# Kernel optimization log

Hardware: AMD Instinct MI355X
Metric: run time of the kernel (lower is better)

## Reference

```python
import jax, jax.numpy as jnp
import numpy as np

N_NODES = 100000
N_EDGES = 1600000
IN_FEAT = 64
OUT_FEAT = 64
NUM_RELS = 8


def setup_inputs() -> dict:
    key = jax.random.key(0)
    k1, k2, k3, k4, k5, k6 = jax.random.split(key, 6)
    feat = jax.random.normal(k1, (N_NODES, IN_FEAT), dtype=jnp.float32)
    norm = jax.random.uniform(k2, (N_EDGES, 1), dtype=jnp.float32)
    # nn.init.uniform_(weight, -1/sqrt(in_feat), 1/sqrt(in_feat))
    bound = 1.0 / np.sqrt(IN_FEAT)
    weight = jax.random.uniform(k3, (NUM_RELS, IN_FEAT, OUT_FEAT), dtype=jnp.float32,
                                minval=-bound, maxval=bound)
    etypes = jax.random.randint(k4, (N_EDGES,), 0, NUM_RELS, dtype=jnp.int64 if jax.config.jax_enable_x64 else jnp.int32)
    src = jax.random.randint(k5, (N_EDGES,), 0, N_NODES, dtype=jnp.int32)
    dst = jax.random.randint(k6, (N_EDGES,), 0, N_NODES, dtype=jnp.int32)
    return {"feat": feat, "norm": norm, "weight": weight,
            "etypes": etypes, "src": src, "dst": dst}


def reference(feat, norm, weight, etypes, src, dst):
    # Original: per-relation grouped matmul on gathered src features, scale by
    # norm, scatter-sum to dst. Matmul distributes over the gather, so we
    # transform all N node features by all R relation weights once (dense GEMM),
    # then gather the right (relation, src) row per edge — same math, fully
    # vectorized, avoids per-edge [in,out] weight gathers.
    transformed = jnp.einsum('ni,rio->rno', feat, weight)   # [R, N, out]
    msg = transformed[etypes, src]                           # [E, out]
    msg = msg * norm                                         # norm broadcasts [E,1]
    out = jax.ops.segment_sum(msg, dst, num_segments=feat.shape[0])  # [N, out]
    return out
```

## Files before the change

kernel.cpp:

```cpp
#include <hip/hip_runtime.h>
#include <hip/hip_bf16.h>

#define N_NODES 100000
#define N_EDGES 1600000
#define IN_FEAT 64
#define OUT_FEAT 64
#define NUM_RELS 8

#define BSHIFT 7
#define BSZ 128
#define NB ((N_NODES + BSZ - 1) / BSZ)
#define CHUNK 4096
#define NCHUNK ((N_EDGES + CHUNK - 1) / CHUNK)
#define PSTR 392
#define MAXBUCK 2944

typedef __attribute__((ext_vector_type(8))) short short8;
typedef __attribute__((ext_vector_type(8))) unsigned short ushort8;
typedef __attribute__((ext_vector_type(4))) float f32x4;

static __device__ __forceinline__ unsigned short f2bf(float x) {
    unsigned u = __float_as_uint(x);
    unsigned r = (u + 0x7FFFu + ((u >> 16) & 1u)) >> 16;
    return (unsigned short)r;
}
static __device__ __forceinline__ float bf2f(unsigned short h) {
    return __uint_as_float(((unsigned)h) << 16);
}
static __device__ __forceinline__ float bflo(unsigned v) { return __uint_as_float(v << 16); }
static __device__ __forceinline__ float bfhi(unsigned v) { return __uint_as_float(v & 0xFFFF0000u); }

__global__ __launch_bounds__(256) void k_prep(const float* __restrict__ W,
                                              unsigned short* __restrict__ Wt) {
    __shared__ float Wl[64 * 64];
    const int r = blockIdx.x, t = threadIdx.x;
    #pragma unroll
    for (int it = 0; it < 16; ++it) {
        int idx = it * 256 + t;
        Wl[idx] = W[(size_t)r * 4096 + idx];
    }
    __syncthreads();
    const int o = t >> 2, iq = t & 3;
    unsigned short tmp[16];
    #pragma unroll
    for (int k = 0; k < 16; ++k) tmp[k] = f2bf(Wl[(iq * 16 + k) * 64 + o]);
    ushort8* dst = (ushort8*)(Wt + ((size_t)r * 64 + o) * 64 + iq * 16);
    dst[0] = *(ushort8*)&tmp[0];
    dst[1] = *(ushort8*)&tmp[8];
}

__global__ __launch_bounds__(256) void k_transform(const float* __restrict__ feat,
                                                   const unsigned short* __restrict__ Wt,
                                                   unsigned short* __restrict__ trb) {
    __shared__ unsigned short Ft[64 * 72];
    __shared__ unsigned short Wtl[64 * 72];
    const int tid = threadIdx.x;
    const int n0b = blockIdx.x * 64;
    const int lane = tid & 63, w = tid >> 6;
    const int lr = lane & 15, lg = lane >> 4;

    #pragma unroll
    for (int it = 0; it < 4; ++it) {
        int m = it * 256 + tid;
        int row = m >> 4, c4 = m & 15;
        int gn = n0b + row;
        float4 v = make_float4(0.f, 0.f, 0.f, 0.f);
        if (gn < N_NODES) v = *(const float4*)(feat + (size_t)gn * IN_FEAT + c4 * 4);
        ushort4 sv;
        sv.x = f2bf(v.x); sv.y = f2bf(v.y); sv.z = f2bf(v.z); sv.w = f2bf(v.w);
        *(ushort4*)&Ft[row * 72 + c4 * 4] = sv;
    }

    for (int rel = 0; rel < NUM_RELS; ++rel) {
        __syncthreads();
        #pragma unroll
        for (int it = 0; it < 2; ++it) {
            int m = it * 256 + tid;
            int row = m >> 3, kq = m & 7;
            *(ushort8*)&Wtl[row * 72 + kq * 8] =
                *(const ushort8*)(Wt + (size_t)rel * 4096 + m * 8);
        }
        __syncthreads();

        short8 a0 = *(const short8*)&Ft[(16 * w + lr) * 72 + lg * 8];
        short8 a1 = *(const short8*)&Ft[(16 * w + lr) * 72 + 32 + lg * 8];

        #pragma unroll
        for (int nt = 0; nt < 4; ++nt) {
            short8 b0 = *(const short8*)&Wtl[(nt * 16 + lr) * 72 + lg * 8];
            short8 b1 = *(const short8*)&Wtl[(nt * 16 + lr) * 72 + 32 + lg * 8];
            f32x4 acc = {0.f, 0.f, 0.f, 0.f};
            acc = __builtin_amdgcn_mfma_f32_16x16x32_bf16(a0, b0, acc, 0, 0, 0);
            acc = __builtin_amdgcn_mfma_f32_16x16x32_bf16(a1, b1, acc, 0, 0, 0);
            #pragma unroll
            for (int j = 0; j < 4; ++j) {
                int row = n0b + 16 * w + lg * 4 + j;
                if (row < N_NODES)
                    trb[((size_t)rel * N_NODES + row) * OUT_FEAT + nt * 16 + lr] = f2bf(acc[j]);
            }
        }
    }
}

__device__ __forceinline__ int block_scan1024(int* arr, int* tmp) {
    const int t = threadIdx.x;
    const int i0 = t * 4;
    int v0 = arr[i0], v1 = arr[i0 + 1], v2 = arr[i0 + 2], v3 = arr[i0 + 3];
    int s = v0 + v1 + v2 + v3;
    tmp[t] = s;
    __syncthreads();
    for (int off = 1; off < 256; off <<= 1) {
        int x = (t >= off) ? tmp[t - off] : 0;
        __syncthreads();
        tmp[t] += x;
        __syncthreads();
    }
    int excl = tmp[t] - s;
    int total = tmp[255];
    arr[i0]     = excl;
    arr[i0 + 1] = excl + v0;
    arr[i0 + 2] = excl + v0 + v1;
    arr[i0 + 3] = excl + v0 + v1 + v2;
    __syncthreads();
    return total;
}

__global__ __launch_bounds__(256) void k_bhist(const int* __restrict__ dst,
                                               int* __restrict__ cnt_kb) {
    __shared__ int h[NB];
    const int k = blockIdx.x, t = threadIdx.x;
    for (int i = t; i < NB; i += 256) h[i] = 0;
    __syncthreads();
    const int e0 = k * CHUNK;
    #pragma unroll
    for (int i = 0; i < 16; ++i) {
        int e = e0 + t + i * 256;
        if (e < N_EDGES) atomicAdd(&h[dst[e] >> BSHIFT], 1);
    }
    __syncthreads();
    for (int i = t; i < NB; i += 256) cnt_kb[(size_t)k * NB + i] = h[i];
}

__global__ __launch_bounds__(256) void k_scan_bucket(const int* __restrict__ cnt_kb,
                                                     int* __restrict__ poff,
                                                     int* __restrict__ btot) {
    __shared__ int arr[1024];
    __shared__ int tmp[256];
    const int b = blockIdx.x, t = threadIdx.x;
    for (int i = t; i < 1024; i += 256)
        arr[i] = (i < NCHUNK) ? cnt_kb[(size_t)i * NB + b] : 0;
    __syncthreads();
    int total = block_scan1024(arr, tmp);
    for (int i = t; i < NCHUNK; i += 256) poff[(size_t)b * PSTR + i] = arr[i];
    if (t == 0) btot[b] = total;
}

__global__ __launch_bounds__(256) void k_scan_tot(const int* __restrict__ btot,
                                                  int* __restrict__ bbase) {
    __shared__ int arr[1024];
    __shared__ int tmp[256];
    const int t = threadIdx.x;
    for (int i = t; i < 1024; i += 256) arr[i] = (i < NB) ? btot[i] : 0;
    __syncthreads();
    block_scan1024(arr, tmp);
    for (int i = t; i < NB; i += 256) bbase[i] = arr[i];
    if (t == 0) bbase[NB] = N_EDGES;
}

__global__ __launch_bounds__(256) void k_bin(const int* __restrict__ etypes,
                                             const int* __restrict__ src,
                                             const int* __restrict__ dst,
                                             const float* __restrict__ norm,
                                             const int* __restrict__ poff,
                                             const int* __restrict__ bbase,
                                             int2* __restrict__ payload) {
    __shared__ int hist[1024];
    __shared__ int tmp[256];
    __shared__ int lcur[NB];
    __shared__ int goff[NB];
    __shared__ int2 ordered[CHUNK];
    __shared__ unsigned short bkt_of[CHUNK];
    const int k = blockIdx.x, t = threadIdx.x;
    const int e0 = k * CHUNK;
    const int cnt = min(CHUNK, N_EDGES - e0);

    for (int i = t; i < 1024; i += 256) hist[i] = 0;
    __syncthreads();
    #pragma unroll
    for (int i = 0; i < 16; ++i) {
        int e = e0 + t + i * 256;
        if (e < N_EDGES) atomicAdd(&hist[dst[e] >> BSHIFT], 1);
    }
    __syncthreads();
    block_scan1024(hist, tmp);
    for (int i = t; i < NB; i += 256) {
        int lb = hist[i];
        lcur[i] = lb;
        goff[i] = bbase[i] + poff[(size_t)i * PSTR + k] - lb;
    }
    __syncthreads();
    #pragma unroll
    for (int i = 0; i < 16; ++i) {
        int e = e0 + t + i * 256;
        if (e < N_EDGES) {
            int d = dst[e];
            int b = d >> BSHIFT;
            int pos = atomicAdd(&lcur[b], 1);
            int rowid = etypes[e] * N_NODES + src[e];
            ordered[pos] = make_int2(rowid | ((d & (BSZ - 1)) << 20), __float_as_int(norm[e]));
            bkt_of[pos] = (unsigned short)b;
        }
    }
    __syncthreads();
    for (int j = t; j < cnt; j += 256) {
        int b = bkt_of[j];
        payload[goff[b] + j] = ordered[j];
    }
}

__global__ __launch_bounds__(512) void k_agg(const unsigned short* __restrict__ trb,
                                             const int2* __restrict__ payload,
                                             const int* __restrict__ bbase,
                                             float* __restrict__ out) {
    __shared__ int2 pseg[MAXBUCK];
    __shared__ unsigned short sidx[MAXBUCK];
    __shared__ int cnt128[BSZ];
    __shared__ int scan_tmp[BSZ];
    __shared__ int ncur[BSZ];
    __shared__ int nbase[BSZ + 1];
    const int b = blockIdx.x, t = threadIdx.x;

    const int s0 = bbase[b], s1 = bbase[b + 1];
    const int cntb = s1 - s0;
    const int cstage = min(cntb, MAXBUCK);

    if (t < BSZ) cnt128[t] = 0;
    __syncthreads();

    for (int i = t; i < cstage; i += 512) {
        int2 p = payload[s0 + i];
        pseg[i] = p;
        atomicAdd(&cnt128[(p.x >> 20) & 127], 1);
    }
    __syncthreads();

    if (t < BSZ) scan_tmp[t] = cnt128[t];
    __syncthreads();
    for (int off = 1; off < BSZ; off <<= 1) {
        int x = 0;
        if (t < BSZ && t >= off) x = scan_tmp[t - off];
        __syncthreads();
        if (t < BSZ) scan_tmp[t] += x;
        __syncthreads();
    }
    if (t < BSZ) {
        int inc = scan_tmp[t];
        int exc = inc - cnt128[t];
        nbase[t] = exc;
        ncur[t] = exc;
        if (t == BSZ - 1) nbase[BSZ] = inc;
    }
    __syncthreads();

    for (int i = t; i < cstage; i += 512) {
        int ld = (pseg[i].x >> 20) & 127;
        int pos = atomicAdd(&ncur[ld], 1);
        sidx[pos] = (unsigned short)i;
    }
    __syncthreads();

    const int gg = t >> 3;
    const int q  = t & 7;
    const int n0g = b << BSHIFT;

    #pragma unroll
    for (int rr = 0; rr < 2; ++rr) {
        int r = gg + rr * 64;
        int j0 = nbase[r], j1 = nbase[r + 1];
        float a0 = 0.f, a1 = 0.f, a2 = 0.f, a3 = 0.f;
        float a4 = 0.f, a5 = 0.f, a6 = 0.f, a7 = 0.f;
        int j = j0;
        for (; j + 1 < j1; j += 2) {
            int2 pa = pseg[sidx[j]];
            int2 pb = pseg[sidx[j + 1]];
            uint4 ua = *(const uint4*)(trb + (size_t)(pa.x & 0xFFFFF) * OUT_FEAT + (q << 3));
            uint4 ub = *(const uint4*)(trb + (size_t)(pb.x & 0xFFFFF) * OUT_FEAT + (q << 3));
            float na = __int_as_float(pa.y);
            float nb_ = __int_as_float(pb.y);
            a0 += bflo(ua.x) * na; a1 += bfhi(ua.x) * na;
            a2 += bflo(ua.y) * na; a3 += bfhi(ua.y) * na;
            a4 += bflo(ua.z) * na; a5 += bfhi(ua.z) * na;
            a6 += bflo(ua.w) * na; a7 += bfhi(ua.w) * na;
            a0 += bflo(ub.x) * nb_; a1 += bfhi(ub.x) * nb_;
            a2 += bflo(ub.y) * nb_; a3 += bfhi(ub.y) * nb_;
            a4 += bflo(ub.z) * nb_; a5 += bfhi(ub.z) * nb_;
            a6 += bflo(ub.w) * nb_; a7 += bfhi(ub.w) * nb_;
        }
        if (j < j1) {
            int2 p = pseg[sidx[j]];
            uint4 u = *(const uint4*)(trb + (size_t)(p.x & 0xFFFFF) * OUT_FEAT + (q << 3));
            float nv = __int_as_float(p.y);
            a0 += bflo(u.x) * nv; a1 += bfhi(u.x) * nv;
            a2 += bflo(u.y) * nv; a3 += bfhi(u.y) * nv;
            a4 += bflo(u.z) * nv; a5 += bfhi(u.z) * nv;
            a6 += bflo(u.w) * nv; a7 += bfhi(u.w) * nv;
        }
        int n = n0g + r;
        if (n < N_NODES) {
            float* op = out + (size_t)n * OUT_FEAT + (q << 3);
            *(float4*)op       = make_float4(a0, a1, a2, a3);
            *(float4*)(op + 4) = make_float4(a4, a5, a6, a7);
        }
    }

    if (cntb > MAXBUCK) {
        __syncthreads();
        for (int i = MAXBUCK + t; i < cntb; i += 512) {
            int2 p = payload[s0 + i];
            int row = p.x & 0xFFFFF;
            int n = n0g + ((p.x >> 20) & 127);
            float nv = __int_as_float(p.y);
            if (n < N_NODES)
                for (int c = 0; c < OUT_FEAT; ++c)
                    atomicAdd(&out[(size_t)n * OUT_FEAT + c],
                              bf2f(trb[(size_t)row * OUT_FEAT + c]) * nv);
        }
    }
}

__global__ __launch_bounds__(256) void k_scatter(const unsigned short* __restrict__ trb,
                                                 const float* __restrict__ norm,
                                                 const int* __restrict__ etypes,
                                                 const int* __restrict__ src,
                                                 const int* __restrict__ dst,
                                                 float* __restrict__ out) {
    int gid = blockIdx.x * 256 + threadIdx.x;
    int e = gid >> 4;
    int q = gid & 15;
    if (e >= N_EDGES) return;
    float nv = norm[e];
    const unsigned short* rp = trb + ((size_t)etypes[e] * N_NODES + src[e]) * OUT_FEAT + q * 4;
    ushort4 u = *(const ushort4*)rp;
    float* op = out + (size_t)dst[e] * OUT_FEAT + q * 4;
    atomicAdd(op + 0, bf2f(u.x) * nv);
    atomicAdd(op + 1, bf2f(u.y) * nv);
    atomicAdd(op + 2, bf2f(u.z) * nv);
    atomicAdd(op + 3, bf2f(u.w) * nv);
}

__global__ __launch_bounds__(256) void k_direct(const float* __restrict__ feat,
                                                const float* __restrict__ W,
                                                const float* __restrict__ norm,
                                                const int* __restrict__ etypes,
                                                const int* __restrict__ src,
                                                const int* __restrict__ dst,
                                                float* __restrict__ out) {
    int gid = blockIdx.x * 256 + threadIdx.x;
    int e = gid >> 4;
    int q = gid & 15;
    if (e >= N_EDGES) return;
    float nv = norm[e];
    const float* fs = feat + (size_t)src[e] * IN_FEAT;
    const float* wp = W + (size_t)etypes[e] * 4096 + q * 4;
    float ax = 0.f, ay = 0.f, az = 0.f, aw = 0.f;
    #pragma unroll 8
    for (int i = 0; i < IN_FEAT; ++i) {
        float f = fs[i];
        float4 w = *(const float4*)(wp + i * OUT_FEAT);
        ax += f * w.x; ay += f * w.y; az += f * w.z; aw += f * w.w;
    }
    float* op = out + (size_t)dst[e] * OUT_FEAT + q * 4;
    atomicAdd(op + 0, ax * nv);
    atomicAdd(op + 1, ay * nv);
    atomicAdd(op + 2, az * nv);
    atomicAdd(op + 3, aw * nv);
}

extern "C" void kernel_launch(void* const* d_in, const int* in_sizes, int n_in,
                              void* d_out, int out_size, void* d_ws, size_t ws_size,
                              hipStream_t stream) {
    const float* feat   = (const float*)d_in[0];
    const float* norm   = (const float*)d_in[1];
    const float* W      = (const float*)d_in[2];
    const int*   etypes = (const int*)d_in[3];
    const int*   src    = (const int*)d_in[4];
    const int*   dst    = (const int*)d_in[5];
    float* out = (float*)d_out;

    const int ntiles = (N_NODES + 63) / 64;
    const int nscat  = (N_EDGES * 16) / 256;

    const size_t sz_tr    = (size_t)NUM_RELS * N_NODES * OUT_FEAT * 2;
    const size_t sz_wt    = (size_t)NUM_RELS * 64 * 64 * 2;
    const size_t sz_cnt   = (((size_t)NCHUNK * NB * 4) + 255) & ~(size_t)255;
    const size_t sz_poff  = (((size_t)NB * PSTR * 4) + 255) & ~(size_t)255;
    const size_t sz_btot  = 3328;
    const size_t sz_bbase = 3328;
    const size_t sz_pay   = (size_t)N_EDGES * 8;

    char* p = (char*)d_ws;
    unsigned short* trb = (unsigned short*)p;  p += sz_tr;
    unsigned short* wt  = (unsigned short*)p;  p += sz_wt;
    int*  cnt_kb  = (int*)p;                   p += sz_cnt;
    int*  poff    = (int*)p;                   p += sz_poff;
    int*  btot    = (int*)p;                   p += sz_btot;
    int*  bbase   = (int*)p;                   p += sz_bbase;
    int2* payload = (int2*)p;                  p += sz_pay;
    const size_t need = (size_t)(p - (char*)d_ws);

    if (ws_size >= need) {
        k_prep       <<<NUM_RELS, 256, 0, stream>>>(W, wt);
        k_transform  <<<ntiles, 256, 0, stream>>>(feat, wt, trb);
        k_bhist      <<<NCHUNK, 256, 0, stream>>>(dst, cnt_kb);
        k_scan_bucket<<<NB,     256, 0, stream>>>(cnt_kb, poff, btot);
        k_scan_tot   <<<1,      256, 0, stream>>>(btot, bbase);
        k_bin        <<<NCHUNK, 256, 0, stream>>>(etypes, src, dst, norm, poff, bbase, payload);
        k_agg        <<<NB,     512, 0, stream>>>(trb, payload, bbase, out);
    } else if (ws_size >= sz_tr + sz_wt) {
        hipMemsetAsync(d_out, 0, (size_t)out_size * sizeof(float), stream);
        k_prep     <<<NUM_RELS, 256, 0, stream>>>(W, wt);
        k_transform<<<ntiles, 256, 0, stream>>>(feat, wt, trb);
        k_scatter  <<<nscat, 256, 0, stream>>>(trb, norm, etypes, src, dst, out);
    } else {
        hipMemsetAsync(d_out, 0, (size_t)out_size * sizeof(float), stream);
        k_direct<<<nscat, 256, 0, stream>>>(feat, W, norm, etypes, src, dst, out);
    }
}
```

Baseline: 112.1 us.

## Aggregate raw features per relation then apply weights via MFMA in aggregation

Drops the precomputed per-relation transformed feature table (8×N×64 bf16). Each destination bucket now sums norm-scaled bf16 source features per (relation, node), writes the sums to shared memory, and multiplies them by each relation's weight with MFMA, accumulating in registers. This removes the large transform write and replaces gathers from an 8x larger table with gathers from a compact bf16 feature array. In exchange it adds per-relation barriers, a 1024-key sort instead of a 128-key one, and an extra bf16 rounding of the partial sums.

Result: slower. 162.2 us (+44.7%).

```diff
diff --git a/kernel.cpp b/kernel.cpp
--- a/kernel.cpp
+++ b/kernel.cpp
@@ -49,57 +49,16 @@
     dst[1] = *(ushort8*)&tmp[8];
 }
 
-__global__ __launch_bounds__(256) void k_transform(const float* __restrict__ feat,
-                                                   const unsigned short* __restrict__ Wt,
-                                                   unsigned short* __restrict__ trb) {
-    __shared__ unsigned short Ft[64 * 72];
-    __shared__ unsigned short Wtl[64 * 72];
-    const int tid = threadIdx.x;
-    const int n0b = blockIdx.x * 64;
-    const int lane = tid & 63, w = tid >> 6;
-    const int lr = lane & 15, lg = lane >> 4;
-
-    #pragma unroll
-    for (int it = 0; it < 4; ++it) {
-        int m = it * 256 + tid;
-        int row = m >> 4, c4 = m & 15;
-        int gn = n0b + row;
-        float4 v = make_float4(0.f, 0.f, 0.f, 0.f);
-        if (gn < N_NODES) v = *(const float4*)(feat + (size_t)gn * IN_FEAT + c4 * 4);
-        ushort4 sv;
-        sv.x = f2bf(v.x); sv.y = f2bf(v.y); sv.z = f2bf(v.z); sv.w = f2bf(v.w);
-        *(ushort4*)&Ft[row * 72 + c4 * 4] = sv;
-    }
-
-    for (int rel = 0; rel < NUM_RELS; ++rel) {
-        __syncthreads();
-        #pragma unroll
-        for (int it = 0; it < 2; ++it) {
-            int m = it * 256 + tid;
-            int row = m >> 3, kq = m & 7;
-            *(ushort8*)&Wtl[row * 72 + kq * 8] =
-                *(const ushort8*)(Wt + (size_t)rel * 4096 + m * 8);
-        }
-        __syncthreads();
-
-        short8 a0 = *(const short8*)&Ft[(16 * w + lr) * 72 + lg * 8];
-        short8 a1 = *(const short8*)&Ft[(16 * w + lr) * 72 + 32 + lg * 8];
-
-        #pragma unroll
-        for (int nt = 0; nt < 4; ++nt) {
-            short8 b0 = *(const short8*)&Wtl[(nt * 16 + lr) * 72 + lg * 8];
-            short8 b1 = *(const short8*)&Wtl[(nt * 16 + lr) * 72 + 32 + lg * 8];
-            f32x4 acc = {0.f, 0.f, 0.f, 0.f};
-            acc = __builtin_amdgcn_mfma_f32_16x16x32_bf16(a0, b0, acc, 0, 0, 0);
-            acc = __builtin_amdgcn_mfma_f32_16x16x32_bf16(a1, b1, acc, 0, 0, 0);
-            #pragma unroll
-            for (int j = 0; j < 4; ++j) {
-                int row = n0b + 16 * w + lg * 4 + j;
-                if (row < N_NODES)
-                    trb[((size_t)rel * N_NODES + row) * OUT_FEAT + nt * 16 + lr] = f2bf(acc[j]);
-            }
-        }
-    }
+__global__ __launch_bounds__(256) void k_featb(const float* __restrict__ feat,
+                                               unsigned short* __restrict__ featb) {
+    int i = blockIdx.x * 256 + threadIdx.x;
+    if (i >= N_NODES * 8) return;
+    float4 v0 = ((const float4*)feat)[(size_t)i * 2];
+    float4 v1 = ((const float4*)feat)[(size_t)i * 2 + 1];
+    ushort8 pw;
+    pw[0] = f2bf(v0.x); pw[1] = f2bf(v0.y); pw[2] = f2bf(v0.z); pw[3] = f2bf(v0.w);
+    pw[4] = f2bf(v1.x); pw[5] = f2bf(v1.y); pw[6] = f2bf(v1.z); pw[7] = f2bf(v1.w);
+    ((ushort8*)featb)[i] = pw;
 }
 
 __device__ __forceinline__ int block_scan1024(int* arr, int* tmp) {
@@ -206,8 +165,8 @@
             int d = dst[e];
             int b = d >> BSHIFT;
             int pos = atomicAdd(&lcur[b], 1);
-            int rowid = etypes[e] * N_NODES + src[e];
-            ordered[pos] = make_int2(rowid | ((d & (BSZ - 1)) << 20), __float_as_int(norm[e]));
+            int pack = src[e] | ((d & (BSZ - 1)) << 17) | (etypes[e] << 24);
+            ordered[pos] = make_int2(pack, __float_as_int(norm[e]));
             bkt_of[pos] = (unsigned short)b;
         }
     }
@@ -218,98 +177,148 @@
     }
 }
 
-__global__ __launch_bounds__(512) void k_agg(const unsigned short* __restrict__ trb,
-                                             const int2* __restrict__ payload,
-                                             const int* __restrict__ bbase,
-                                             float* __restrict__ out) {
+__global__ __launch_bounds__(512, 6) void k_agg(const unsigned short* __restrict__ featb,
+                                                const unsigned short* __restrict__ Wt,
+                                                const float* __restrict__ Worig,
+                                                const float* __restrict__ featf,
+                                                const int2* __restrict__ payload,
+                                                const int* __restrict__ bbase,
+                                                float* __restrict__ out) {
     __shared__ int2 pseg[MAXBUCK];
     __shared__ unsigned short sidx[MAXBUCK];
-    __shared__ int cnt128[BSZ];
-    __shared__ int scan_tmp[BSZ];
-    __shared__ int ncur[BSZ];
-    __shared__ int nbase[BSZ + 1];
+    __shared__ int nbase[1025];
+    __shared__ __align__(16) unsigned char uu[128 * 72 * 2];
+    unsigned short* P = (unsigned short*)uu;
+    int* cnt  = (int*)uu;
+    int* ncur = (int*)(uu + 4096);
+    int* stmp = (int*)(uu + 8192);
+
     const int b = blockIdx.x, t = threadIdx.x;
-
     const int s0 = bbase[b], s1 = bbase[b + 1];
     const int cntb = s1 - s0;
     const int cstage = min(cntb, MAXBUCK);
 
-    if (t < BSZ) cnt128[t] = 0;
+    for (int i = t; i < 1024; i += 512) cnt[i] = 0;
     __syncthreads();
 
     for (int i = t; i < cstage; i += 512) {
         int2 p = payload[s0 + i];
         pseg[i] = p;
-        atomicAdd(&cnt128[(p.x >> 20) & 127], 1);
-    }
-    __syncthreads();
-
-    if (t < BSZ) scan_tmp[t] = cnt128[t];
-    __syncthreads();
-    for (int off = 1; off < BSZ; off <<= 1) {
-        int x = 0;
-        if (t < BSZ && t >= off) x = scan_tmp[t - off];
-        __syncthreads();
-        if (t < BSZ) scan_tmp[t] += x;
-        __syncthreads();
-    }
-    if (t < BSZ) {
-        int inc = scan_tmp[t];
-        int exc = inc - cnt128[t];
-        nbase[t] = exc;
-        ncur[t] = exc;
-        if (t == BSZ - 1) nbase[BSZ] = inc;
+        atomicAdd(&cnt[(p.x >> 17) & 1023], 1);
+    }
+    __syncthreads();
+
+    {
+        int v0 = cnt[2 * t], v1 = cnt[2 * t + 1];
+        int s = v0 + v1;
+        stmp[t] = s;
+        __syncthreads();
+        for (int off = 1; off < 512; off <<= 1) {
+            int x = (t >= off) ? stmp[t - off] : 0;
+            __syncthreads();
+            stmp[t] += x;
+            __syncthreads();
+        }
+        int excl = stmp[t] - s;
+        nbase[2 * t]     = excl;
+        nbase[2 * t + 1] = excl + v0;
+        ncur[2 * t]      = excl;
+        ncur[2 * t + 1]  = excl + v0;
+        if (t == 0) nbase[1024] = cstage;
     }
     __syncthreads();
 
     for (int i = t; i < cstage; i += 512) {
-        int ld = (pseg[i].x >> 20) & 127;
-        int pos = atomicAdd(&ncur[ld], 1);
+        int key = (pseg[i].x >> 17) & 1023;
+        int pos = atomicAdd(&ncur[key], 1);
         sidx[pos] = (unsigned short)i;
     }
     __syncthreads();
 
-    const int gg = t >> 3;
-    const int q  = t & 7;
+    const int lane = t & 63, w = t >> 6;
+    const int lr = lane & 15, lg = lane >> 4;
+    const int gg = t >> 3, q = t & 7;
     const int n0g = b << BSHIFT;
-
-    #pragma unroll
-    for (int rr = 0; rr < 2; ++rr) {
-        int r = gg + rr * 64;
-        int j0 = nbase[r], j1 = nbase[r + 1];
-        float a0 = 0.f, a1 = 0.f, a2 = 0.f, a3 = 0.f;
-        float a4 = 0.f, a5 = 0.f, a6 = 0.f, a7 = 0.f;
-        int j = j0;
-        for (; j + 1 < j1; j += 2) {
-            int2 pa = pseg[sidx[j]];
-            int2 pb = pseg[sidx[j + 1]];
-            uint4 ua = *(const uint4*)(trb + (size_t)(pa.x & 0xFFFFF) * OUT_FEAT + (q << 3));
-            uint4 ub = *(const uint4*)(trb + (size_t)(pb.x & 0xFFFFF) * OUT_FEAT + (q << 3));
-            float na = __int_as_float(pa.y);
-            float nb_ = __int_as_float(pb.y);
-            a0 += bflo(ua.x) * na; a1 += bfhi(ua.x) * na;
-            a2 += bflo(ua.y) * na; a3 += bfhi(ua.y) * na;
-            a4 += bflo(ua.z) * na; a5 += bfhi(ua.z) * na;
-            a6 += bflo(ua.w) * na; a7 += bfhi(ua.w) * na;
-            a0 += bflo(ub.x) * nb_; a1 += bfhi(ub.x) * nb_;
-            a2 += bflo(ub.y) * nb_; a3 += bfhi(ub.y) * nb_;
-            a4 += bflo(ub.z) * nb_; a5 += bfhi(ub.z) * nb_;
-            a6 += bflo(ub.w) * nb_; a7 += bfhi(ub.w) * nb_;
-        }
-        if (j < j1) {
-            int2 p = pseg[sidx[j]];
-            uint4 u = *(const uint4*)(trb + (size_t)(p.x & 0xFFFFF) * OUT_FEAT + (q << 3));
-            float nv = __int_as_float(p.y);
-            a0 += bflo(u.x) * nv; a1 += bfhi(u.x) * nv;
-            a2 += bflo(u.y) * nv; a3 += bfhi(u.y) * nv;
-            a4 += bflo(u.z) * nv; a5 += bfhi(u.z) * nv;
-            a6 += bflo(u.w) * nv; a7 += bfhi(u.w) * nv;
-        }
-        int n = n0g + r;
-        if (n < N_NODES) {
-            float* op = out + (size_t)n * OUT_FEAT + (q << 3);
-            *(float4*)op       = make_float4(a0, a1, a2, a3);
-            *(float4*)(op + 4) = make_float4(a4, a5, a6, a7);
+    const short* Wts = (const short*)Wt;
+
+    f32x4 c0 = {0.f, 0.f, 0.f, 0.f};
+    f32x4 c1 = {0.f, 0.f, 0.f, 0.f};
+    f32x4 c2 = {0.f, 0.f, 0.f, 0.f};
+    f32x4 c3 = {0.f, 0.f, 0.f, 0.f};
+
+    for (int r = 0; r < NUM_RELS; ++r) {
+        #pragma unroll
+        for (int rr = 0; rr < 2; ++rr) {
+            int nodeid = gg + rr * 64;
+            int key = (r << 7) | nodeid;
+            int j0 = nbase[key], j1 = nbase[key + 1];
+            float s0_ = 0.f, s1_ = 0.f, s2_ = 0.f, s3_ = 0.f;
+            float s4_ = 0.f, s5_ = 0.f, s6_ = 0.f, s7_ = 0.f;
+            int j = j0;
+            for (; j + 1 < j1; j += 2) {
+                int2 pa = pseg[sidx[j]];
+                int2 pb = pseg[sidx[j + 1]];
+                uint4 ua = *(const uint4*)(featb + (size_t)(pa.x & 0x1FFFF) * 64 + (q << 3));
+                uint4 ub = *(const uint4*)(featb + (size_t)(pb.x & 0x1FFFF) * 64 + (q << 3));
+                float na = __int_as_float(pa.y), nb_ = __int_as_float(pb.y);
+                s0_ += bflo(ua.x) * na; s1_ += bfhi(ua.x) * na;
+                s2_ += bflo(ua.y) * na; s3_ += bfhi(ua.y) * na;
+                s4_ += bflo(ua.z) * na; s5_ += bfhi(ua.z) * na;
+                s6_ += bflo(ua.w) * na; s7_ += bfhi(ua.w) * na;
+                s0_ += bflo(ub.x) * nb_; s1_ += bfhi(ub.x) * nb_;
+                s2_ += bflo(ub.y) * nb_; s3_ += bfhi(ub.y) * nb_;
+                s4_ += bflo(ub.z) * nb_; s5_ += bfhi(ub.z) * nb_;
+                s6_ += bflo(ub.w) * nb_; s7_ += bfhi(ub.w) * nb_;
+            }
+            if (j < j1) {
+                int2 p = pseg[sidx[j]];
+                uint4 u = *(const uint4*)(featb + (size_t)(p.x & 0x1FFFF) * 64 + (q << 3));
+                float nv = __int_as_float(p.y);
+                s0_ += bflo(u.x) * nv; s1_ += bfhi(u.x) * nv;
+                s2_ += bflo(u.y) * nv; s3_ += bfhi(u.y) * nv;
+                s4_ += bflo(u.z) * nv; s5_ += bfhi(u.z) * nv;
+                s6_ += bflo(u.w) * nv; s7_ += bfhi(u.w) * nv;
+            }
+            ushort8 pw;
+            pw[0] = f2bf(s0_); pw[1] = f2bf(s1_); pw[2] = f2bf(s2_); pw[3] = f2bf(s3_);
+            pw[4] = f2bf(s4_); pw[5] = f2bf(s5_); pw[6] = f2bf(s6_); pw[7] = f2bf(s7_);
+            *(ushort8*)&P[nodeid * 72 + (q << 3)] = pw;
+        }
+        __syncthreads();
+
+        short8 a0 = *(const short8*)&P[(16 * w + lr) * 72 + lg * 8];
+        short8 a1 = *(const short8*)&P[(16 * w + lr) * 72 + 32 + lg * 8];
+        {
+            short8 b0, b1;
+            b0 = *(const short8*)(Wts + ((size_t)r * 64 + 0 * 16 + lr) * 64 + lg * 8);
+            b1 = *(const short8*)(Wts + ((size_t)r * 64 + 0 * 16 + lr) * 64 + 32 + lg * 8);
+            c0 = __builtin_amdgcn_mfma_f32_16x16x32_bf16(a0, b0, c0, 0, 0, 0);
+            c0 = __builtin_amdgcn_mfma_f32_16x16x32_bf16(a1, b1, c0, 0, 0, 0);
+            b0 = *(const short8*)(Wts + ((size_t)r * 64 + 1 * 16 + lr) * 64 + lg * 8);
+            b1 = *(const short8*)(Wts + ((size_t)r * 64 + 1 * 16 + lr) * 64 + 32 + lg * 8);
+            c1 = __builtin_amdgcn_mfma_f32_16x16x32_bf16(a0, b0, c1, 0, 0, 0);
+            c1 = __builtin_amdgcn_mfma_f32_16x16x32_bf16(a1, b1, c1, 0, 0, 0);
+            b0 = *(const short8*)(Wts + ((size_t)r * 64 + 2 * 16 + lr) * 64 + lg * 8);
+            b1 = *(const short8*)(Wts + ((size_t)r * 64 + 2 * 16 + lr) * 64 + 32 + lg * 8);
+            c2 = __builtin_amdgcn_mfma_f32_16x16x32_bf16(a0, b0, c2, 0, 0, 0);
+            c2 = __builtin_amdgcn_mfma_f32_16x16x32_bf16(a1, b1, c2, 0, 0, 0);
+            b0 = *(const short8*)(Wts + ((size_t)r * 64 + 3 * 16 + lr) * 64 + lg * 8);
+            b1 = *(const short8*)(Wts + ((size_t)r * 64 + 3 * 16 + lr) * 64 + 32 + lg * 8);
+            c3 = __builtin_amdgcn_mfma_f32_16x16x32_bf16(a0, b0, c3, 0, 0, 0);
+            c3 = __builtin_amdgcn_mfma_f32_16x16x32_bf16(a1, b1, c3, 0, 0, 0);
+        }
+        __syncthreads();
+    }
+
+    #pragma unroll
+    for (int j = 0; j < 4; ++j) {
+        int row = n0g + 16 * w + lg * 4 + j;
+        if (row < N_NODES) {
+            float* op = out + (size_t)row * OUT_FEAT;
+            op[0 * 16 + lr] = c0[j];
+            op[1 * 16 + lr] = c1[j];
+            op[2 * 16 + lr] = c2[j];
+            op[3 * 16 + lr] = c3[j];
         }
     }
 
@@ -317,35 +326,20 @@
         __syncthreads();
         for (int i = MAXBUCK + t; i < cntb; i += 512) {
             int2 p = payload[s0 + i];
-            int row = p.x & 0xFFFFF;
-            int n = n0g + ((p.x >> 20) & 127);
+            int srcn = p.x & 0x1FFFF;
+            int rel  = (p.x >> 24) & 7;
+            int n    = n0g + ((p.x >> 17) & 127);
             float nv = __int_as_float(p.y);
-            if (n < N_NODES)
-                for (int c = 0; c < OUT_FEAT; ++c)
-                    atomicAdd(&out[(size_t)n * OUT_FEAT + c],
-                              bf2f(trb[(size_t)row * OUT_FEAT + c]) * nv);
-        }
-    }
-}
-
-__global__ __launch_bounds__(256) void k_scatter(const unsigned short* __restrict__ trb,
-                                                 const float* __restrict__ norm,
-                                                 const int* __restrict__ etypes,
-                                                 const int* __restrict__ src,
-                                                 const int* __restrict__ dst,
-                                                 float* __restrict__ out) {
-    int gid = blockIdx.x * 256 + threadIdx.x;
-    int e = gid >> 4;
-    int q = gid & 15;
-    if (e >= N_EDGES) return;
-    float nv = norm[e];
-    const unsigned short* rp = trb + ((size_t)etypes[e] * N_NODES + src[e]) * OUT_FEAT + q * 4;
-    ushort4 u = *(const ushort4*)rp;
-    float* op = out + (size_t)dst[e] * OUT_FEAT + q * 4;
-    atomicAdd(op + 0, bf2f(u.x) * nv);
-    atomicAdd(op + 1, bf2f(u.y) * nv);
-    atomicAdd(op + 2, bf2f(u.z) * nv);
-    atomicAdd(op + 3, bf2f(u.w) * nv);
+            if (n < N_NODES) {
+                for (int c = 0; c < OUT_FEAT; ++c) {
+                    float s = 0.f;
+                    for (int i2 = 0; i2 < IN_FEAT; ++i2)
+                        s += featf[(size_t)srcn * 64 + i2] * Worig[((size_t)rel * 64 + i2) * 64 + c];
+                    atomicAdd(&out[(size_t)n * 64 + c], s * nv);
+                }
+            }
+        }
+    }
 }
 
 __global__ __launch_bounds__(256) void k_direct(const float* __restrict__ feat,
@@ -387,10 +381,9 @@
     const int*   dst    = (const int*)d_in[5];
     float* out = (float*)d_out;
 
-    const int ntiles = (N_NODES + 63) / 64;
-    const int nscat  = (N_EDGES * 16) / 256;
-
-    const size_t sz_tr    = (size_t)NUM_RELS * N_NODES * OUT_FEAT * 2;
+    const int nscat = (N_EDGES * 16) / 256;
+
+    const size_t sz_featb = (size_t)N_NODES * IN_FEAT * 2;
     const size_t sz_wt    = (size_t)NUM_RELS * 64 * 64 * 2;
     const size_t sz_cnt   = (((size_t)NCHUNK * NB * 4) + 255) & ~(size_t)255;
     const size_t sz_poff  = (((size_t)NB * PSTR * 4) + 255) & ~(size_t)255;
@@ -399,28 +392,23 @@
     const size_t sz_pay   = (size_t)N_EDGES * 8;
 
     char* p = (char*)d_ws;
-    unsigned short* trb = (unsigned short*)p;  p += sz_tr;
-    unsigned short* wt  = (unsigned short*)p;  p += sz_wt;
-    int*  cnt_kb  = (int*)p;                   p += sz_cnt;
-    int*  poff    = (int*)p;                   p += sz_poff;
-    int*  btot    = (int*)p;                   p += sz_btot;
-    int*  bbase   = (int*)p;                   p += sz_bbase;
-    int2* payload = (int2*)p;                  p += sz_pay;
+    unsigned short* featb = (unsigned short*)p;  p += sz_featb;
+    unsigned short* wt    = (unsigned short*)p;  p += sz_wt;
+    int*  cnt_kb  = (int*)p;                     p += sz_cnt;
+    int*  poff    = (int*)p;                     p += sz_poff;
+    int*  btot    = (int*)p;                     p += sz_btot;
+    int*  bbase   = (int*)p;                     p += sz_bbase;
+    int2* payload = (int2*)p;                    p += sz_pay;
     const size_t need = (size_t)(p - (char*)d_ws);
 
     if (ws_size >= need) {
         k_prep       <<<NUM_RELS, 256, 0, stream>>>(W, wt);
-        k_transform  <<<ntiles, 256, 0, stream>>>(feat, wt, trb);
+        k_featb      <<<(N_NODES * 8 + 255) / 256, 256, 0, stream>>>(feat, featb);
         k_bhist      <<<NCHUNK, 256, 0, stream>>>(dst, cnt_kb);
         k_scan_bucket<<<NB,     256, 0, stream>>>(cnt_kb, poff, btot);
         k_scan_tot   <<<1,      256, 0, stream>>>(btot, bbase);
         k_bin        <<<NCHUNK, 256, 0, stream>>>(etypes, src, dst, norm, poff, bbase, payload);
-        k_agg        <<<NB,     512, 0, stream>>>(trb, payload, bbase, out);
-    } else if (ws_size >= sz_tr + sz_wt) {
-        hipMemsetAsync(d_out, 0, (size_t)out_size * sizeof(float), stream);
-        k_prep     <<<NUM_RELS, 256, 0, stream>>>(W, wt);
-        k_transform<<<ntiles, 256, 0, stream>>>(feat, wt, trb);
-        k_scatter  <<<nscat, 256, 0, stream>>>(trb, norm, etypes, src, dst, out);
+        k_agg        <<<NB,     512, 0, stream>>>(featb, wt, W, feat, payload, bbase, out);
     } else {
         hipMemsetAsync(d_out, 0, (size_t)out_size * sizeof(float), stream);
         k_direct<<<nscat, 256, 0, stream>>>(feat, W, norm, etypes, src, dst, out);
```
